# Kernel tuning notes

Hardware: AMD Instinct MI355X
Metric: run time of the kernel (lower is better)

## Reference

```python
import jax, jax.numpy as jnp
import numpy as np

DIM = 1024
NUM_PATTERNS = 8192
B, S = 2, 4096


def setup_inputs() -> dict:
    key = jax.random.key(0)
    k1, k2, k3 = jax.random.split(key, 3)
    scale = 1.0 / np.sqrt(DIM)
    x = jax.random.normal(k1, (B, S, DIM), dtype=jnp.float32)
    # nn.Linear default init ~ U(-1/sqrt(in), 1/sqrt(in)); normal*scale is fine for a baseline
    w_q = jax.random.normal(k2, (DIM, DIM), dtype=jnp.float32) * scale
    xi = jax.random.normal(k3, (NUM_PATTERNS, DIM), dtype=jnp.float32) * scale
    beta = jnp.float32(1.0 / np.sqrt(DIM))
    return {"x": x, "w_q": w_q, "xi": xi, "beta": beta}


def reference(x, w_q, xi, beta):
    # q = x @ w_q.T  (torch F.linear convention: weight is [out, in])
    q = jnp.einsum("bsd,ed->bse", x, w_q)
    # logits = beta * q @ xi.T  -> [B, S, P]
    logits = beta * jnp.einsum("bsd,pd->bsp", q, xi)
    attn = jax.nn.softmax(logits, axis=-1)
    # retrieve patterns: attn @ xi -> [B, S, dim]
    return jnp.einsum("bsp,pd->bsd", attn, xi)
```

## Files before the change

kernel.cpp:

```cpp
#include <hip/hip_runtime.h>


typedef __attribute__((ext_vector_type(8))) int int8v;
typedef __attribute__((ext_vector_type(4))) float f32x4;

#define NDIM 1024
#define NPAT 8192
#define NROW 8192

__device__ __forceinline__ unsigned f8pack4(float a, float b, float c, float d) {
  int w = __builtin_amdgcn_cvt_pk_fp8_f32(a, b, 0, false);
  w = __builtin_amdgcn_cvt_pk_fp8_f32(c, d, w, true);
  return (unsigned)w;
}
__device__ __forceinline__ unsigned char f8b(float v) {
  return (unsigned char)(__builtin_amdgcn_cvt_pk_fp8_f32(v, v, 0, false) & 0xff);
}
__device__ __forceinline__ int sig(int c) {
  return (c & 64) | ((c & 15) << 2) | ((c >> 4) & 3);
}

__device__ __forceinline__ void gload_lds16(const void* g, void* l) {
  __builtin_amdgcn_global_load_lds(
      (const __attribute__((address_space(1))) unsigned char*)g,
      (__attribute__((address_space(3))) unsigned char*)l,
      16, 0, 0);
}

__device__ __forceinline__ int8v lds_read32(const char* p) {
  return *(const int8v*)__builtin_assume_aligned(p, 32);
}


__global__ void cast_f8(const float* __restrict__ in,
                        unsigned* __restrict__ out, float scale, int n4) {
  int i = blockIdx.x * blockDim.x + threadIdx.x;
  if (i < n4) {
    float4 v = ((const float4*)in)[i];
    out[i] = f8pack4(v.x * scale, v.y * scale, v.z * scale, v.w * scale);
  }
}

__global__ void xi_prep8(const float* __restrict__ xi,
                         unsigned char* __restrict__ xi8,
                         unsigned char* __restrict__ xit8,
                         float* __restrict__ colsum) {
  __shared__ float t[32][33];
  __shared__ float cs[8][32];
  int tx = threadIdx.x, ty = threadIdx.y;
  int d0 = blockIdx.x * 32, p0 = blockIdx.y * 32;
  int d = d0 + tx;
  int di = (d & ~127) + sig(d & 127);
  float psum = 0.f;
#pragma unroll
  for (int j = 0; j < 32; j += 8) {
    float v = xi[(long)(p0 + ty + j) * NDIM + d];
    t[ty + j][tx] = v;
    psum += v;
    xi8[(long)(p0 + ty + j) * NDIM + di] = f8b(32.f * v);
  }
  cs[ty][tx] = psum;
  __syncthreads();
  if (ty == 0) {
    float s = 0.f;
#pragma unroll
    for (int k = 0; k < 8; ++k) s += cs[k][tx];
    atomicAdd(&colsum[d0 + tx], s);
  }
  int p = p0 + tx;
  int pi = (p & ~127) + sig(p & 127);
#pragma unroll
  for (int j = 0; j < 32; j += 8)
    xit8[(long)(d0 + ty + j) * NPAT + pi] = f8b(32.f * t[tx][ty + j]);
}


template <int MODE, int WM, int WN>
__launch_bounds__(WM* WN * 64, 2)
__global__ void gemm_f8(const unsigned char* __restrict__ A,
                        const unsigned char* __restrict__ B,
                        void* __restrict__ Cv, int N, int K,
                        const float* __restrict__ beta_ptr,
                        const float* __restrict__ rowsum,
                        const float* __restrict__ colsum,
                        float* __restrict__ rowsum_out) {
  constexpr int NW = WM * WN;
  constexpr int BM = WM * 64;
  constexpr int BN = WN * 128;
  constexpr int NGA = BM / 8;
  constexpr int NG = (BM + BN) / 8;
  constexpr int G = NG / NW;
  __shared__ unsigned char smem[(BM + BN) * 128];
  char* Asm = (char*)smem;
  char* Bsm = (char*)smem + BM * 128;

  const int tid = threadIdx.x;
  const int wave = tid >> 6;
  const int lane = tid & 63;
  const int wm = wave / WN, wn = wave % WN;
  const int quad = lane >> 4, ln = lane & 15;

  const long row0 = (long)blockIdx.y * BM;
  const long col0 = (long)blockIdx.x * BN;
  const unsigned char* baseA = A + row0 * (long)K;
  const unsigned char* baseB = B + col0 * (long)K;

  const int r_in = lane >> 3;
  const int csl = lane & 7;
  const int cg = ((((csl >> 1) ^ (r_in & 3)) << 1) | (csl & 1));
  const unsigned char* gsrc[G];
  char* ldst[G];
#pragma unroll
  for (int p = 0; p < G; ++p) {
    int g = wave * G + p;
    if (g < NGA) {
      gsrc[p] = baseA + (g * 8 + r_in) * (long)K + cg * 16;
      ldst[p] = Asm + g * 1024;
    } else {
      gsrc[p] = baseB + ((g - NGA) * 8 + r_in) * (long)K + cg * 16;
      ldst[p] = Bsm + (g - NGA) * 1024;
    }
  }

  const int ps = (quad ^ (ln & 3)) * 32;
  const int base_a = (wm * 64 + ln) * 128 + ps;
  const int base_b = (wn * 128 + ln) * 128 + ps;

  f32x4 acc[4][8] = {};

  for (int kt = 0; kt < K; kt += 128) {
#pragma unroll
    for (int p = 0; p < G; ++p) gload_lds16(gsrc[p], ldst[p]);
#pragma unroll
    for (int p = 0; p < G; ++p) gsrc[p] += 128;
    __syncthreads();

    int8v af[4];
#pragma unroll
    for (int mt = 0; mt < 4; ++mt)
      af[mt] = lds_read32(Asm + base_a + mt * 2048);
#pragma unroll
    for (int nt = 0; nt < 8; ++nt) {
      int8v bf = lds_read32(Bsm + base_b + nt * 2048);
#pragma unroll
      for (int mt = 0; mt < 4; ++mt)
        acc[mt][nt] = __builtin_amdgcn_mfma_scale_f32_16x16x128_f8f6f4(
            af[mt], bf, acc[mt][nt], 0, 0, 0, 0x7f7f7f7f, 0, 0x7f7f7f7f);
    }
    __syncthreads();
  }

  if (MODE == 0) {
    unsigned* C32 = (unsigned*)Cv;
    const float s = 1.0f / 32.0f;
#pragma unroll
    for (int mt = 0; mt < 4; ++mt)
#pragma unroll
      for (int r = 0; r < 4; ++r) {
        long row = row0 + wm * 64 + mt * 16 + quad * 4 + r;
        long w0 = row * (N >> 2) + (col0 >> 2) + wn * 32;
        C32[w0 + ln] = f8pack4(acc[mt][0][r] * s, acc[mt][1][r] * s,
                               acc[mt][2][r] * s, acc[mt][3][r] * s);
        C32[w0 + 16 + ln] = f8pack4(acc[mt][4][r] * s, acc[mt][5][r] * s,
                                    acc[mt][6][r] * s, acc[mt][7][r] * s);
      }
  } else if (MODE == 1) {
    unsigned* C32 = (unsigned*)Cv;
    const float bs = beta_ptr[0] * (1.0f / 32.0f);
#pragma unroll
    for (int mt = 0; mt < 4; ++mt)
#pragma unroll
      for (int r = 0; r < 4; ++r) {
        long row = row0 + wm * 64 + mt * 16 + quad * 4 + r;
        float e[8];
        float s = 0.f;
#pragma unroll
        for (int nt = 0; nt < 8; ++nt) {
          e[nt] = (__expf(bs * acc[mt][nt][r]) - 1.0f) * 32.f;
          s += e[nt];
        }
        long w0 = row * (N >> 2) + (col0 >> 2) + wn * 32;
        C32[w0 + ln] = f8pack4(e[0], e[1], e[2], e[3]);
        C32[w0 + 16 + ln] = f8pack4(e[4], e[5], e[6], e[7]);
        s += __shfl_xor(s, 1, 64);
        s += __shfl_xor(s, 2, 64);
        s += __shfl_xor(s, 4, 64);
        s += __shfl_xor(s, 8, 64);
        if (ln == 0) atomicAdd(&rowsum_out[row], s);
      }
  } else {
    float* C = (float*)Cv;
#pragma unroll
    for (int mt = 0; mt < 4; ++mt)
#pragma unroll
      for (int r = 0; r < 4; ++r) {
        long row = row0 + wm * 64 + mt * 16 + quad * 4 + r;
        float inv = 1.0f / (8192.0f + rowsum[row] * (1.0f / 32.0f));
#pragma unroll
        for (int nt = 0; nt < 8; ++nt) {
          long col = col0 + wn * 128 + nt * 16 + ln;
          C[row * N + col] =
              (acc[mt][nt][r] * (1.0f / 1024.0f) + colsum[col]) * inv;
        }
      }
  }
}


extern "C" void kernel_launch(void* const* d_in, const int* in_sizes, int n_in,
                              void* d_out, int out_size, void* d_ws,
                              size_t ws_size, hipStream_t stream) {
  const float* x    = (const float*)d_in[0];
  const float* wq   = (const float*)d_in[1];
  const float* xi   = (const float*)d_in[2];
  const float* beta = (const float*)d_in[3];
  float* out = (float*)d_out;

  char* ws = (char*)d_ws;
  const size_t MB = 1024 * 1024;
  unsigned char* x8   = (unsigned char*)(ws);
  unsigned char* wq8  = (unsigned char*)(ws + 8 * MB);
  unsigned char* q8   = (unsigned char*)(ws + 9 * MB);
  unsigned char* xi8  = (unsigned char*)(ws + 17 * MB);
  unsigned char* xit8 = (unsigned char*)(ws + 25 * MB);
  float*         rs   = (float*)(ws + 33 * MB);
  float*         csum = (float*)(ws + 33 * MB + 32768);
  unsigned char* E8   = (unsigned char*)(ws + 34 * MB);

  hipMemsetAsync(rs, 0, 36864, stream);

  cast_f8<<<(NROW * NDIM / 4) / 256, 256, 0, stream>>>(
      x, (unsigned*)x8, 1.0f, NROW * NDIM / 4);
  cast_f8<<<(NDIM * NDIM / 4) / 256, 256, 0, stream>>>(
      wq, (unsigned*)wq8, 32.0f, NDIM * NDIM / 4);
  xi_prep8<<<dim3(NDIM / 32, NPAT / 32), dim3(32, 8), 0, stream>>>(
      xi, xi8, xit8, csum);

  gemm_f8<0, 1, 2><<<dim3(NDIM / 256, NROW / 64), 128, 0, stream>>>(
      x8, wq8, q8, NDIM, NDIM, nullptr, nullptr, nullptr, nullptr);

  gemm_f8<1, 2, 2><<<dim3(NPAT / 256, NROW / 128), 256, 0, stream>>>(
      q8, xi8, E8, NPAT, NDIM, beta, nullptr, nullptr, rs);

  gemm_f8<2, 1, 2><<<dim3(NDIM / 256, NROW / 64), 128, 0, stream>>>(
      E8, xit8, out, NDIM, NPAT, nullptr, rs, csum, nullptr);
}
```

Before: 331.8 us.

## Split-K the final GEMM with atomic accumulation and retile the projection GEMM

The attention-times-patterns GEMM is split four ways along its 8192-long K dimension via a third grid axis. Partial results are combined with float atomic adds into an output buffer that is zeroed first, and the column-sum bias term is added only by the first split. The projection GEMM switches to 128x128 tiles with 256 threads. This aims to raise the number of blocks and occupancy for the long-K GEMM, at the cost of a full output memset, atomic read-modify-write traffic, and nondeterministic summation order.

```diff
diff --git a/kernel.cpp b/kernel.cpp
--- a/kernel.cpp
+++ b/kernel.cpp
@@ -75,18 +75,18 @@
 }
 
 
-template <int MODE, int WM, int WN>
+template <int MODE, int WM, int WN, int NT>
 __launch_bounds__(WM* WN * 64, 2)
 __global__ void gemm_f8(const unsigned char* __restrict__ A,
                         const unsigned char* __restrict__ B,
-                        void* __restrict__ Cv, int N, int K,
+                        void* __restrict__ Cv, int N, int Ktot, int KC,
                         const float* __restrict__ beta_ptr,
                         const float* __restrict__ rowsum,
                         const float* __restrict__ colsum,
                         float* __restrict__ rowsum_out) {
   constexpr int NW = WM * WN;
   constexpr int BM = WM * 64;
-  constexpr int BN = WN * 128;
+  constexpr int BN = WN * NT * 16;
   constexpr int NGA = BM / 8;
   constexpr int NG = (BM + BN) / 8;
   constexpr int G = NG / NW;
@@ -102,8 +102,9 @@
 
   const long row0 = (long)blockIdx.y * BM;
   const long col0 = (long)blockIdx.x * BN;
-  const unsigned char* baseA = A + row0 * (long)K;
-  const unsigned char* baseB = B + col0 * (long)K;
+  const long koff = (long)blockIdx.z * KC;
+  const unsigned char* baseA = A + row0 * (long)Ktot + koff;
+  const unsigned char* baseB = B + col0 * (long)Ktot + koff;
 
   const int r_in = lane >> 3;
   const int csl = lane & 7;
@@ -114,21 +115,21 @@
   for (int p = 0; p < G; ++p) {
     int g = wave * G + p;
     if (g < NGA) {
-      gsrc[p] = baseA + (g * 8 + r_in) * (long)K + cg * 16;
+      gsrc[p] = baseA + (g * 8 + r_in) * (long)Ktot + cg * 16;
       ldst[p] = Asm + g * 1024;
     } else {
-      gsrc[p] = baseB + ((g - NGA) * 8 + r_in) * (long)K + cg * 16;
+      gsrc[p] = baseB + ((g - NGA) * 8 + r_in) * (long)Ktot + cg * 16;
       ldst[p] = Bsm + (g - NGA) * 1024;
     }
   }
 
   const int ps = (quad ^ (ln & 3)) * 32;
   const int base_a = (wm * 64 + ln) * 128 + ps;
-  const int base_b = (wn * 128 + ln) * 128 + ps;
-
-  f32x4 acc[4][8] = {};
-
-  for (int kt = 0; kt < K; kt += 128) {
+  const int base_b = (wn * (NT * 16) + ln) * 128 + ps;
+
+  f32x4 acc[4][NT] = {};
+
+  for (int kt = 0; kt < KC; kt += 128) {
 #pragma unroll
     for (int p = 0; p < G; ++p) gload_lds16(gsrc[p], ldst[p]);
 #pragma unroll
@@ -140,7 +141,7 @@
     for (int mt = 0; mt < 4; ++mt)
       af[mt] = lds_read32(Asm + base_a + mt * 2048);
 #pragma unroll
-    for (int nt = 0; nt < 8; ++nt) {
+    for (int nt = 0; nt < NT; ++nt) {
       int8v bf = lds_read32(Bsm + base_b + nt * 2048);
 #pragma unroll
       for (int mt = 0; mt < 4; ++mt)
@@ -158,11 +159,9 @@
 #pragma unroll
       for (int r = 0; r < 4; ++r) {
         long row = row0 + wm * 64 + mt * 16 + quad * 4 + r;
-        long w0 = row * (N >> 2) + (col0 >> 2) + wn * 32;
-        C32[w0 + ln] = f8pack4(acc[mt][0][r] * s, acc[mt][1][r] * s,
-                               acc[mt][2][r] * s, acc[mt][3][r] * s);
-        C32[w0 + 16 + ln] = f8pack4(acc[mt][4][r] * s, acc[mt][5][r] * s,
-                                    acc[mt][6][r] * s, acc[mt][7][r] * s);
+        C32[row * (N >> 2) + (col0 >> 2) + wn * 16 + ln] =
+            f8pack4(acc[mt][0][r] * s, acc[mt][1][r] * s, acc[mt][2][r] * s,
+                    acc[mt][3][r] * s);
       }
   } else if (MODE == 1) {
     unsigned* C32 = (unsigned*)Cv;
@@ -172,16 +171,17 @@
 #pragma unroll
       for (int r = 0; r < 4; ++r) {
         long row = row0 + wm * 64 + mt * 16 + quad * 4 + r;
-        float e[8];
+        float e[NT];
         float s = 0.f;
 #pragma unroll
-        for (int nt = 0; nt < 8; ++nt) {
+        for (int nt = 0; nt < NT; ++nt) {
           e[nt] = (__expf(bs * acc[mt][nt][r]) - 1.0f) * 32.f;
           s += e[nt];
         }
-        long w0 = row * (N >> 2) + (col0 >> 2) + wn * 32;
+        long w0 = row * (N >> 2) + (col0 >> 2) + wn * (NT * 4);
         C32[w0 + ln] = f8pack4(e[0], e[1], e[2], e[3]);
-        C32[w0 + 16 + ln] = f8pack4(e[4], e[5], e[6], e[7]);
+        if (NT == 8)
+          C32[w0 + 16 + ln] = f8pack4(e[4], e[5], e[6], e[7]);
         s += __shfl_xor(s, 1, 64);
         s += __shfl_xor(s, 2, 64);
         s += __shfl_xor(s, 4, 64);
@@ -190,6 +190,7 @@
       }
   } else {
     float* C = (float*)Cv;
+    const bool first = (blockIdx.z == 0);
 #pragma unroll
     for (int mt = 0; mt < 4; ++mt)
 #pragma unroll
@@ -197,10 +198,11 @@
         long row = row0 + wm * 64 + mt * 16 + quad * 4 + r;
         float inv = 1.0f / (8192.0f + rowsum[row] * (1.0f / 32.0f));
 #pragma unroll
-        for (int nt = 0; nt < 8; ++nt) {
-          long col = col0 + wn * 128 + nt * 16 + ln;
-          C[row * N + col] =
-              (acc[mt][nt][r] * (1.0f / 1024.0f) + colsum[col]) * inv;
+        for (int nt = 0; nt < NT; ++nt) {
+          long col = col0 + wn * (NT * 16) + nt * 16 + ln;
+          float v = acc[mt][nt][r] * (1.0f / 1024.0f) * inv;
+          if (first) v += colsum[col] * inv;
+          unsafeAtomicAdd(&C[row * N + col], v);
         }
       }
   }
@@ -228,6 +230,7 @@
   unsigned char* E8   = (unsigned char*)(ws + 34 * MB);
 
   hipMemsetAsync(rs, 0, 36864, stream);
+  hipMemsetAsync(out, 0, (size_t)NROW * NDIM * 4, stream);
 
   cast_f8<<<(NROW * NDIM / 4) / 256, 256, 0, stream>>>(
       x, (unsigned*)x8, 1.0f, NROW * NDIM / 4);
@@ -236,12 +239,12 @@
   xi_prep8<<<dim3(NDIM / 32, NPAT / 32), dim3(32, 8), 0, stream>>>(
       xi, xi8, xit8, csum);
 
-  gemm_f8<0, 1, 2><<<dim3(NDIM / 256, NROW / 64), 128, 0, stream>>>(
-      x8, wq8, q8, NDIM, NDIM, nullptr, nullptr, nullptr, nullptr);
-
-  gemm_f8<1, 2, 2><<<dim3(NPAT / 256, NROW / 128), 256, 0, stream>>>(
-      q8, xi8, E8, NPAT, NDIM, beta, nullptr, nullptr, rs);
-
-  gemm_f8<2, 1, 2><<<dim3(NDIM / 256, NROW / 64), 128, 0, stream>>>(
-      E8, xit8, out, NDIM, NPAT, nullptr, rs, csum, nullptr);
-}
+  gemm_f8<0, 2, 2, 4><<<dim3(NDIM / 128, NROW / 128), 256, 0, stream>>>(
+      x8, wq8, q8, NDIM, NDIM, NDIM, nullptr, nullptr, nullptr, nullptr);
+
+  gemm_f8<1, 2, 2, 8><<<dim3(NPAT / 256, NROW / 128), 256, 0, stream>>>(
+      q8, xi8, E8, NPAT, NDIM, NDIM, beta, nullptr, nullptr, rs);
+
+  gemm_f8<2, 2, 2, 8><<<dim3(NDIM / 256, NROW / 128, 4), 256, 0, stream>>>(
+      E8, xit8, out, NDIM, NPAT, NPAT / 4, nullptr, rs, csum, nullptr);
+}
```

After: 391.9 us. 18.1% more time.
